# Performance work log

Measured on AMD Instinct MI355X. Metric: run time of the kernel, lower is better.

## Reference

```python
import jax, jax.numpy as jnp
import numpy as np

B, T, D, F = 32, 512, 512, 256
K = 3
MEL_MAX = 4096
EPS = 1e-5


def _xavier(key, shape, fan_in, fan_out):
    lim = float(np.sqrt(6.0 / (fan_in + fan_out)))
    return jax.random.uniform(key, shape, jnp.float32, -lim, lim)


def setup_inputs() -> dict:
    key = jax.random.key(0)
    ks = jax.random.split(key, 6)
    x = jax.random.normal(ks[0], (B, T, D), jnp.float32)
    target = jax.random.randint(ks[1], (B, T), 0, 8)  # per-token durations
    # conv weights stored as [K, I, O] (lax 'WIO'); torch xavier on [O,I,K]: fan_in=I*K, fan_out=O*K
    w1 = _xavier(ks[2], (K, D, F), D * K, F * K)
    b1 = jnp.zeros((F,), jnp.float32)
    g1 = jnp.ones((F,), jnp.float32)
    be1 = jnp.zeros((F,), jnp.float32)
    w2 = _xavier(ks[3], (K, F, F), F * K, F * K)
    b2 = jnp.zeros((F,), jnp.float32)
    g2 = jnp.ones((F,), jnp.float32)
    be2 = jnp.zeros((F,), jnp.float32)
    wl = _xavier(ks[4], (F, 1), F, 1)
    bl = jnp.zeros((1,), jnp.float32)
    return dict(x=x, target=target, mel_max_length=MEL_MAX,
                w1=w1, b1=b1, g1=g1, be1=be1,
                w2=w2, b2=b2, g2=g2, be2=be2, wl=wl, bl=bl)


def _layer_norm(h, g, b):
    mu = jnp.mean(h, axis=-1, keepdims=True)
    var = jnp.mean(jnp.square(h - mu), axis=-1, keepdims=True)
    return (h - mu) * jax.lax.rsqrt(var + EPS) * g + b


def _conv1d(h, w, b):
    # h: [B,T,C_in], w: [K,C_in,C_out]; torch padding=1 with K=3 == SAME
    out = jax.lax.conv_general_dilated(h, w, (1,), 'SAME',
                                       dimension_numbers=('NWC', 'WIO', 'NWC'))
    return out + b


def reference(x, target, mel_max_length, w1, b1, g1, be1, w2, b2, g2, be2, wl, bl):
    # ---- DurationPredictor (eval: dropout = identity) ----
    h = jax.nn.relu(_layer_norm(_conv1d(x, w1, b1), g1, be1))
    h = jax.nn.relu(_layer_norm(_conv1d(h, w2, b2), g2, be2))
    dur_pred = jax.nn.relu(h @ wl + bl)[..., 0]  # [B, T]

    # ---- LR: ragged expansion of x by `target` durations, padded to mel_max_length ----
    cum = jnp.cumsum(target, axis=1)              # [B, T]
    total = cum[:, -1]                            # [B]
    pos = jnp.arange(mel_max_length)              # [M]
    # frame m maps to token i with cum[i-1] <= m < cum[i]
    idx = jax.vmap(lambda c: jnp.searchsorted(c, pos, side='right'))(cum)  # [B, M]
    idx = jnp.clip(idx, 0, x.shape[1] - 1)
    mask = pos[None, :] < total[:, None]          # [B, M]
    out = jnp.take_along_axis(x, idx[..., None], axis=1) * mask[..., None].astype(x.dtype)
    return (out, dur_pred)
```

## Files before the change

kernel.cpp:

```cpp
#include <hip/hip_runtime.h>
#include <type_traits>

#define B_   32
#define T_   512
#define D_   512
#define F_   256
#define MEL  4096
#define EPS_ 1e-5f

typedef __attribute__((ext_vector_type(8))) short bf16x8;
typedef __attribute__((ext_vector_type(4))) float f32x4;

#define GLL16(gp, lp) \
    __builtin_amdgcn_global_load_lds((const __attribute__((address_space(1))) void*)(gp), \
                                     (__attribute__((address_space(3))) void*)(lp), 16, 0, 0)
#define BARRIER() do { asm volatile("" ::: "memory"); __builtin_amdgcn_s_barrier(); \
                       asm volatile("" ::: "memory"); } while (0)

__device__ inline unsigned short f2bf(float f) {
    unsigned u = __float_as_uint(f);
    unsigned r = (u + 0x7fff + ((u >> 16) & 1)) >> 16;
    return (unsigned short)r;
}

#define PREP_WBLOCKS 2304

__global__ __launch_bounds__(256)
void prep_kernel(const float* __restrict__ w1, const float* __restrict__ w2,
                 const int* __restrict__ tgt,
                 unsigned short* __restrict__ w1T, unsigned short* __restrict__ w2T,
                 int* __restrict__ gidx)
{
    __shared__ int lcum[T_];
    __shared__ int wsum[4];

    int bid = blockIdx.x;
    int tid = threadIdx.x;
    if (bid < PREP_WBLOCKS) {
        int idx = bid * 256 + tid;
        if (idx < 3 * D_ * F_) {
            int kk = idx / F_, f = idx % F_;
            w1T[(size_t)f * (3 * D_) + kk] = f2bf(w1[idx]);
        } else {
            int j = idx - 3 * D_ * F_;
            int kk = j / F_, f = j % F_;
            w2T[(size_t)f * (3 * F_) + kk] = f2bf(w2[j]);
        }
        return;
    }

    int b = bid - PREP_WBLOCKS;
    int t0 = tid * 2;
    int a0 = tgt[b * T_ + t0], a1 = tgt[b * T_ + t0 + 1];
    int lane = tid & 63, w = tid >> 6;
    int v = a0 + a1;
#pragma unroll
    for (int o = 1; o < 64; o <<= 1) { int u = __shfl_up(v, o); if (lane >= o) v += u; }
    if (lane == 63) wsum[w] = v;
    __syncthreads();
    int base = 0;
#pragma unroll
    for (int i = 0; i < 4; ++i) if (i < w) base += wsum[i];
    int incl = base + v;
    lcum[t0]     = incl - a1;
    lcum[t0 + 1] = incl;
    __syncthreads();

    int total = lcum[T_ - 1];
#pragma unroll
    for (int k = 0; k < MEL / 256; ++k) {
        int pos = tid + k * 256;
        int lo = 0, hi = T_;
        while (lo < hi) { int mid = (lo + hi) >> 1; if (lcum[mid] <= pos) lo = mid + 1; else hi = mid; }
        gidx[b * MEL + pos] = (pos < total) ? min(lo, T_ - 1) : -1;
    }
}

template<int IN_D, typename InT, bool FUSE_DUR, int GROWS, int GOFF>
__global__ __launch_bounds__(1024)
void conv_gather_kernel(const InT* __restrict__ x, const unsigned short* __restrict__ wT,
                        const float* __restrict__ bias, const float* __restrict__ gamma,
                        const float* __restrict__ beta, unsigned short* __restrict__ out,
                        const float* __restrict__ wl, const float* __restrict__ bl,
                        float* __restrict__ dur,
                        const float* __restrict__ xf, const int* __restrict__ gidx,
                        float* __restrict__ gout)
{
    constexpr int MT = 64;
    constexpr int KT = 3 * IN_D;
    constexpr int PHASES = KT / 64;
    constexpr int NBAR = 2 + 2 * PHASES + (FUSE_DUR ? 1 : 0);

    __shared__ __align__(16) char xs_raw[(MT + 2) * IN_D * 2];
    __shared__ __align__(16) unsigned short xsB[2 * 16384];
    __shared__ float red[MT][8];
    __shared__ float redD[MT][4];

    const int l = threadIdx.x & 63;

    if (threadIdx.x >= 512) {
        const int gw = (threadIdx.x >> 6) - 8;
        const int rbase = GOFF + blockIdx.x * (GROWS * 8) + gw * GROWS;
        int myidx = (l < GROWS) ? gidx[rbase + l] : -1;
        int done = 0;
        for (int bar = 0; bar < NBAR; ++bar) {
            __builtin_amdgcn_s_barrier();
            int tgt = (int)(((long)(bar + 1) * GROWS) / NBAR);
            for (; done < tgt; ++done) {
                int r = rbase + done;
                int ix = __shfl(myidx, done);
                float4 v0 = make_float4(0.f, 0.f, 0.f, 0.f), v1 = v0;
                if (ix >= 0) {
                    const float* s = xf + ((size_t)(r >> 12) * T_ + ix) * D_ + l * 8;
                    v0 = *reinterpret_cast<const float4*>(s);
                    v1 = *reinterpret_cast<const float4*>(s + 4);
                }
                float* d = gout + (size_t)r * D_ + l * 8;
                *reinterpret_cast<float4*>(d)     = v0;
                *reinterpret_cast<float4*>(d + 4) = v1;
            }
        }
        return;
    }

    const int blocksPerBatch = T_ / MT;
    const int b  = blockIdx.x / blocksPerBatch;
    const int t0 = (blockIdx.x % blocksPerBatch) * MT;
    const int wv = threadIdx.x >> 6;
    const int fg = wv & 3;
    const int rg = wv >> 2;

    constexpr int CH = (MT + 2) * IN_D / 8;
    for (int c = threadIdx.x; c < CH; c += 512) {
        int j  = c / (IN_D / 8);
        int d8 = (c % (IN_D / 8)) * 8;
        int t  = t0 - 1 + j;
        uint4 pk = make_uint4(0u, 0u, 0u, 0u);
        if (t >= 0 && t < T_) {
            if constexpr (std::is_same_v<InT, float>) {
                const float4* src = reinterpret_cast<const float4*>(&x[((size_t)b * T_ + t) * IN_D + d8]);
                float4 a0 = src[0], a1 = src[1];
                pk.x = (unsigned)f2bf(a0.x) | ((unsigned)f2bf(a0.y) << 16);
                pk.y = (unsigned)f2bf(a0.z) | ((unsigned)f2bf(a0.w) << 16);
                pk.z = (unsigned)f2bf(a1.x) | ((unsigned)f2bf(a1.y) << 16);
                pk.w = (unsigned)f2bf(a1.z) | ((unsigned)f2bf(a1.w) << 16);
            } else {
                pk = *reinterpret_cast<const uint4*>(&x[((size_t)b * T_ + t) * IN_D + d8]);
            }
        }
        int byte = ((j * IN_D + d8) * 2) ^ ((j & 7) << 4);
        *reinterpret_cast<uint4*>(&xs_raw[byte]) = pk;
    }

    float bv[4], gv[4], bev[4], wlv[4];
#pragma unroll
    for (int n = 0; n < 4; ++n) {
        int f = fg * 64 + n * 16 + (l & 15);
        bv[n] = bias[f]; gv[n] = gamma[f]; bev[n] = beta[f];
        if constexpr (FUSE_DUR) wlv[n] = wl[f];
    }
    float blv = FUSE_DUR ? bl[0] : 0.f;

    __syncthreads();

    const int sbase = wv * 4;
    auto stageB = [&](int ph, int buf) {
        int p = ph < PHASES ? ph : PHASES - 1;
        unsigned short* lb = &xsB[buf * 16384];
#pragma unroll
        for (int i = 0; i < 4; ++i) {
            int s = sbase + i;
            int c = s * 64 + l;
            int f = c >> 3;
            int kg = (c & 7) ^ (f & 7);
            const unsigned short* src = wT + (size_t)f * KT + p * 64 + kg * 8;
            GLL16(src, lb + s * 512);
        }
    };
    auto loadBfrag = [&](bf16x8* dst, int buf, int kk2) {
#pragma unroll
        for (int n = 0; n < 4; ++n) {
            int f  = fg * 64 + n * 16 + (l & 15);
            int kg = kk2 * 4 + (l >> 4);
            dst[n] = *reinterpret_cast<const bf16x8*>(&xsB[buf * 16384 + f * 64 + ((kg ^ (f & 7)) * 8)]);
        }
    };
    const int k_lane = (l >> 4) * 8;
    auto loadA = [&](bf16x8* dst, int kk) {
        int kp = kk / IN_D;
        int dbase = (kk % IN_D) + k_lane;
#pragma unroll
        for (int m = 0; m < 2; ++m) {
            int j = rg * 32 + m * 16 + (l & 15) + kp;
            int byte = ((j * IN_D + dbase) * 2) ^ ((j & 7) << 4);
            dst[m] = *reinterpret_cast<const bf16x8*>(&xs_raw[byte]);
        }
    };

    f32x4 acc[2][4];
#pragma unroll
    for (int m = 0; m < 2; ++m)
#pragma unroll
        for (int n = 0; n < 4; ++n) acc[m][n] = (f32x4){0.f, 0.f, 0.f, 0.f};

    stageB(0, 0);
    stageB(1, 1);
    for (int p = 0; p < PHASES; ++p) {
        asm volatile("s_waitcnt vmcnt(4)" ::: "memory");
        BARRIER();
        int buf = p & 1;
#pragma unroll
        for (int kk2 = 0; kk2 < 2; ++kk2) {
            int kk = p * 64 + kk2 * 32;
            bf16x8 Bv[4], Av[2];
            loadBfrag(Bv, buf, kk2);
            loadA(Av, kk);
#pragma unroll
            for (int m = 0; m < 2; ++m)
#pragma unroll
                for (int n = 0; n < 4; ++n)
                    acc[m][n] = __builtin_amdgcn_mfma_f32_16x16x32_bf16(Av[m], Bv[n], acc[m][n], 0, 0, 0);
        }
        BARRIER();
        stageB(p + 2, buf);
    }

#pragma unroll
    for (int m = 0; m < 2; ++m)
#pragma unroll
        for (int q = 0; q < 4; ++q) {
            float s = 0.f, s2 = 0.f;
#pragma unroll
            for (int n = 0; n < 4; ++n) {
                float v2 = acc[m][n][q] + bv[n];
                acc[m][n][q] = v2;
                s += v2; s2 += v2 * v2;
            }
#pragma unroll
            for (int o = 1; o < 16; o <<= 1) { s += __shfl_xor(s, o); s2 += __shfl_xor(s2, o); }
            int row = rg * 32 + m * 16 + (l >> 4) * 4 + q;
            if ((l & 15) == 0) { red[row][fg * 2] = s; red[row][fg * 2 + 1] = s2; }
        }
    __syncthreads();

#pragma unroll
    for (int m = 0; m < 2; ++m)
#pragma unroll
        for (int q = 0; q < 4; ++q) {
            int row = rg * 32 + m * 16 + (l >> 4) * 4 + q;
            float s  = red[row][0] + red[row][2] + red[row][4] + red[row][6];
            float s2 = red[row][1] + red[row][3] + red[row][5] + red[row][7];
            float mu  = s * (1.f / F_);
            float var = s2 * (1.f / F_) - mu * mu;
            float rs  = rsqrtf(var + EPS_);
            size_t rbase = ((size_t)(b * T_ + t0 + row)) * F_;
            float part = 0.f;
#pragma unroll
            for (int n = 0; n < 4; ++n) {
                float y = (acc[m][n][q] - mu) * rs * gv[n] + bev[n];
                y = fmaxf(y, 0.f);
                out[rbase + fg * 64 + n * 16 + (l & 15)] = f2bf(y);
                if constexpr (FUSE_DUR) part = fmaf(y, wlv[n], part);
            }
            if constexpr (FUSE_DUR) {
#pragma unroll
                for (int o = 1; o < 16; o <<= 1) part += __shfl_xor(part, o);
                if ((l & 15) == 0) redD[row][fg] = part;
            }
        }

    if constexpr (FUSE_DUR) {
        __syncthreads();
        if (threadIdx.x < MT) {
            float s = redD[threadIdx.x][0] + redD[threadIdx.x][1]
                    + redD[threadIdx.x][2] + redD[threadIdx.x][3] + blv;
            dur[(size_t)b * T_ + t0 + threadIdx.x] = fmaxf(s, 0.f);
        }
    }
}

extern "C" void kernel_launch(void* const* d_in, const int* in_sizes, int n_in,
                              void* d_out, int out_size, void* d_ws, size_t ws_size,
                              hipStream_t stream)
{
    const float* x      = (const float*)d_in[0];
    const int*   target = (const int*)d_in[1];
    const float* w1  = (const float*)d_in[3];
    const float* b1  = (const float*)d_in[4];
    const float* g1  = (const float*)d_in[5];
    const float* be1 = (const float*)d_in[6];
    const float* w2  = (const float*)d_in[7];
    const float* b2  = (const float*)d_in[8];
    const float* g2  = (const float*)d_in[9];
    const float* be2 = (const float*)d_in[10];
    const float* wl  = (const float*)d_in[11];
    const float* bl  = (const float*)d_in[12];

    float* out = (float*)d_out;
    float* dur = out + (size_t)B_ * MEL * D_;

    char* ws = (char*)d_ws;
    unsigned short* w1T = (unsigned short*)ws;         ws += (size_t)F_ * (3 * D_) * 2;
    unsigned short* w2T = (unsigned short*)ws;         ws += (size_t)F_ * (3 * F_) * 2;
    unsigned short* h1  = (unsigned short*)ws;         ws += (size_t)B_ * T_ * F_ * 2;
    unsigned short* h2  = (unsigned short*)ws;         ws += (size_t)B_ * T_ * F_ * 2;
    int*            gidx = (int*)ws;

    prep_kernel<<<PREP_WBLOCKS + B_, 256, 0, stream>>>(w1, w2, target, w1T, w2T, gidx);

    conv_gather_kernel<D_, float, false, 40, 0><<<B_ * (T_ / 64), 1024, 0, stream>>>(
        x, w1T, b1, g1, be1, h1, nullptr, nullptr, nullptr, x, gidx, out);
    conv_gather_kernel<F_, unsigned short, true, 24, 81920><<<B_ * (T_ / 64), 1024, 0, stream>>>(
        h1, w2T, b2, g2, be2, h2, wl, bl, dur, x, gidx, out);
}
```

Before: 108.6 us.

## Interleave gather copies into MFMA warps instead of dedicated gather warps

Removes the eight extra gather-only waves per block and has the eight MFMA waves run the ragged gather copy themselves. Each wave keeps a three-deep software pipeline of gather loads, issued between the conv phases, with hand-tuned vmcnt waits so the gather traffic overlaps the weight staging and MFMA work. The row split between the two conv kernels changes to 48 and 16 rows per wave. This trades the 1024-thread blocks for 512-thread blocks that may fit better per CU, but it adds register pressure and depends on exact vmcnt accounting being correct.

```diff
diff --git a/kernel.cpp b/kernel.cpp
--- a/kernel.cpp
+++ b/kernel.cpp
@@ -16,6 +16,7 @@
                                      (__attribute__((address_space(3))) void*)(lp), 16, 0, 0)
 #define BARRIER() do { asm volatile("" ::: "memory"); __builtin_amdgcn_s_barrier(); \
                        asm volatile("" ::: "memory"); } while (0)
+#define MEMPIN() asm volatile("" ::: "memory")
 
 __device__ inline unsigned short f2bf(float f) {
     unsigned u = __float_as_uint(f);
@@ -76,56 +77,29 @@
     }
 }
 
-template<int IN_D, typename InT, bool FUSE_DUR, int GROWS, int GOFF>
-__global__ __launch_bounds__(1024)
-void conv_gather_kernel(const InT* __restrict__ x, const unsigned short* __restrict__ wT,
-                        const float* __restrict__ bias, const float* __restrict__ gamma,
-                        const float* __restrict__ beta, unsigned short* __restrict__ out,
-                        const float* __restrict__ wl, const float* __restrict__ bl,
-                        float* __restrict__ dur,
-                        const float* __restrict__ xf, const int* __restrict__ gidx,
-                        float* __restrict__ gout)
+template<int IN_D, typename InT, bool FUSE_DUR, int GPHASES, int GBASE>
+__global__ __launch_bounds__(512)
+void conv_mfma_kernel(const InT* __restrict__ x, const unsigned short* __restrict__ wT,
+                      const float* __restrict__ bias, const float* __restrict__ gamma,
+                      const float* __restrict__ beta, unsigned short* __restrict__ out,
+                      const float* __restrict__ wl, const float* __restrict__ bl,
+                      float* __restrict__ dur,
+                      const float* __restrict__ xf, const int* __restrict__ gidx,
+                      float* __restrict__ gout)
 {
     constexpr int MT = 64;
     constexpr int KT = 3 * IN_D;
     constexpr int PHASES = KT / 64;
-    constexpr int NBAR = 2 + 2 * PHASES + (FUSE_DUR ? 1 : 0);
 
     __shared__ __align__(16) char xs_raw[(MT + 2) * IN_D * 2];
     __shared__ __align__(16) unsigned short xsB[2 * 16384];
     __shared__ float red[MT][8];
     __shared__ float redD[MT][4];
 
-    const int l = threadIdx.x & 63;
-
-    if (threadIdx.x >= 512) {
-        const int gw = (threadIdx.x >> 6) - 8;
-        const int rbase = GOFF + blockIdx.x * (GROWS * 8) + gw * GROWS;
-        int myidx = (l < GROWS) ? gidx[rbase + l] : -1;
-        int done = 0;
-        for (int bar = 0; bar < NBAR; ++bar) {
-            __builtin_amdgcn_s_barrier();
-            int tgt = (int)(((long)(bar + 1) * GROWS) / NBAR);
-            for (; done < tgt; ++done) {
-                int r = rbase + done;
-                int ix = __shfl(myidx, done);
-                float4 v0 = make_float4(0.f, 0.f, 0.f, 0.f), v1 = v0;
-                if (ix >= 0) {
-                    const float* s = xf + ((size_t)(r >> 12) * T_ + ix) * D_ + l * 8;
-                    v0 = *reinterpret_cast<const float4*>(s);
-                    v1 = *reinterpret_cast<const float4*>(s + 4);
-                }
-                float* d = gout + (size_t)r * D_ + l * 8;
-                *reinterpret_cast<float4*>(d)     = v0;
-                *reinterpret_cast<float4*>(d + 4) = v1;
-            }
-        }
-        return;
-    }
-
     const int blocksPerBatch = T_ / MT;
     const int b  = blockIdx.x / blocksPerBatch;
     const int t0 = (blockIdx.x % blocksPerBatch) * MT;
+    const int l  = threadIdx.x & 63;
     const int wv = threadIdx.x >> 6;
     const int fg = wv & 3;
     const int rg = wv >> 2;
@@ -161,7 +135,13 @@
     }
     float blv = FUSE_DUR ? bl[0] : 0.f;
 
+    asm volatile("s_waitcnt vmcnt(0)" ::: "memory");
     __syncthreads();
+
+    constexpr int GROWS = 2 * GPHASES;
+    const int rbase = GBASE + (blockIdx.x * 8 + wv) * GROWS;
+    int gidxv = gidx[rbase + min(l, GROWS - 1)];
+    MEMPIN();
 
     const int sbase = wv * 4;
     auto stageB = [&](int ph, int buf) {
@@ -197,16 +177,50 @@
         }
     };
 
+    float4 ga[3][2][2];
+    auto loadSet = [&](int slot, int s) {
+#pragma unroll
+        for (int i = 0; i < 2; ++i) {
+            int li = min(2 * s + i, GROWS - 1);
+            int ix = __shfl(gidxv, li);
+            int r  = rbase + li;
+            const float* src = xf + ((size_t)(r >> 12) * T_ + max(ix, 0)) * D_ + l * 4;
+            ga[slot][i][0] = *reinterpret_cast<const float4*>(src);
+            ga[slot][i][1] = *reinterpret_cast<const float4*>(src + 256);
+        }
+    };
+    auto storeSet = [&](int slot, int s) {
+#pragma unroll
+        for (int i = 0; i < 2; ++i) {
+            int li = 2 * s + i;
+            int ix = __shfl(gidxv, li);
+            int r  = rbase + li;
+            float4 a = ga[slot][i][0], c = ga[slot][i][1];
+            if (ix < 0) { a = make_float4(0.f,0.f,0.f,0.f); c = make_float4(0.f,0.f,0.f,0.f); }
+            float* d = gout + (size_t)r * D_ + l * 4;
+            *reinterpret_cast<float4*>(d)       = a;
+            *reinterpret_cast<float4*>(d + 256) = c;
+        }
+    };
+
     f32x4 acc[2][4];
 #pragma unroll
     for (int m = 0; m < 2; ++m)
 #pragma unroll
         for (int n = 0; n < 4; ++n) acc[m][n] = (f32x4){0.f, 0.f, 0.f, 0.f};
 
-    stageB(0, 0);
-    stageB(1, 1);
+    stageB(0, 0);  MEMPIN();
+    stageB(1, 1);  MEMPIN();
+    loadSet(0, 0); MEMPIN();
+    loadSet(1, 1); MEMPIN();
+    loadSet(2, 2);
+
+#pragma unroll
     for (int p = 0; p < PHASES; ++p) {
-        asm volatile("s_waitcnt vmcnt(4)" ::: "memory");
+        if (p == 0)                asm volatile("s_waitcnt vmcnt(8)"  ::: "memory");
+        else if (p == 1)           asm volatile("s_waitcnt vmcnt(16)" ::: "memory");
+        else if (p < GPHASES + 1)  asm volatile("s_waitcnt vmcnt(12)" ::: "memory");
+        else                       asm volatile("s_waitcnt vmcnt(4)"  ::: "memory");
         BARRIER();
         int buf = p & 1;
 #pragma unroll
@@ -222,6 +236,10 @@
                     acc[m][n] = __builtin_amdgcn_mfma_f32_16x16x32_bf16(Av[m], Bv[n], acc[m][n], 0, 0, 0);
         }
         BARRIER();
+        if (p < GPHASES) {
+            storeSet(p % 3, p);
+            loadSet(p % 3, p + 3);
+        }
         stageB(p + 2, buf);
     }
 
@@ -253,13 +271,13 @@
             float mu  = s * (1.f / F_);
             float var = s2 * (1.f / F_) - mu * mu;
             float rs  = rsqrtf(var + EPS_);
-            size_t rbase = ((size_t)(b * T_ + t0 + row)) * F_;
+            size_t rb2 = ((size_t)(b * T_ + t0 + row)) * F_;
             float part = 0.f;
 #pragma unroll
             for (int n = 0; n < 4; ++n) {
                 float y = (acc[m][n][q] - mu) * rs * gv[n] + bev[n];
                 y = fmaxf(y, 0.f);
-                out[rbase + fg * 64 + n * 16 + (l & 15)] = f2bf(y);
+                out[rb2 + fg * 64 + n * 16 + (l & 15)] = f2bf(y);
                 if constexpr (FUSE_DUR) part = fmaf(y, wlv[n], part);
             }
             if constexpr (FUSE_DUR) {
@@ -308,8 +326,8 @@
 
     prep_kernel<<<PREP_WBLOCKS + B_, 256, 0, stream>>>(w1, w2, target, w1T, w2T, gidx);
 
-    conv_gather_kernel<D_, float, false, 40, 0><<<B_ * (T_ / 64), 1024, 0, stream>>>(
+    conv_mfma_kernel<D_, float, false, 24, 0><<<B_ * (T_ / 64), 512, 0, stream>>>(
         x, w1T, b1, g1, be1, h1, nullptr, nullptr, nullptr, x, gidx, out);
-    conv_gather_kernel<F_, unsigned short, true, 24, 81920><<<B_ * (T_ / 64), 1024, 0, stream>>>(
+    conv_mfma_kernel<F_, unsigned short, true, 8, 98304><<<B_ * (T_ / 64), 512, 0, stream>>>(
         h1, w2T, b2, g2, be2, h2, wl, bl, dur, x, gidx, out);
 }
```

Result: faster. 95.23 us (-12.3%).
